# Kernel tuning notes

Measured on AMD Instinct MI355X. Metric: run time of the kernel, lower is better.

The kernel has to match this reference:

```python
import jax, jax.numpy as jnp
import numpy as np
from functools import partial

B, H, W = 2, 480, 480
C, HALF = 32, 16
L, WN, PAD = 4, 20, 20

def gelu(x):
    return jax.nn.gelu(x, approximate=False)

def setup_inputs() -> dict:
    key = jax.random.key(0)
    ks = jax.random.split(key, 24)
    scale = 1.0 / (C * C)
    d = {}
    d["input_data"] = jax.random.normal(ks[0], (B, H, W, 1), jnp.float32)
    d["src_data"] = jax.random.normal(ks[1], (B, H, W, 3), jnp.float32)
    # input lifting MLP: sizes [5, 16, 32]
    d["in_w1"] = jax.random.normal(ks[2], (5, HALF), jnp.float32) * 0.1
    d["in_b1"] = jnp.zeros((HALF,), jnp.float32)
    d["in_w2"] = jax.random.normal(ks[3], (HALF, C), jnp.float32) * 0.1
    d["in_b2"] = jnp.zeros((C,), jnp.float32)
    # eps lifting MLP: sizes [3, 16, 32]
    d["eps_w1"] = jax.random.normal(ks[4], (3, HALF), jnp.float32) * 0.1
    d["eps_b1"] = jnp.zeros((HALF,), jnp.float32)
    d["eps_w2"] = jax.random.normal(ks[5], (HALF, C), jnp.float32) * 0.1
    d["eps_b2"] = jnp.zeros((C,), jnp.float32)
    # Fourier layer params, stacked over L layers
    d["fw1"] = jax.random.uniform(ks[6], (L, C, C, WN, WN, 2), jnp.float32) * scale
    d["fw2"] = jax.random.uniform(ks[7], (L, C, C, WN, WN, 2), jnp.float32) * scale
    d["conv_w"] = jax.random.normal(ks[8], (L, C, C), jnp.float32) * 0.05
    d["conv_b"] = jnp.zeros((L, C), jnp.float32)
    # projection MLP: sizes [32, 16, 2]
    d["proj_w1"] = jax.random.normal(ks[9], (C, HALF), jnp.float32) * 0.1
    d["proj_b1"] = jnp.zeros((HALF,), jnp.float32)
    d["proj_w2"] = jax.random.normal(ks[10], (HALF, 2), jnp.float32) * 0.1
    d["proj_b2"] = jnp.zeros((2,), jnp.float32)
    # mask conv 3x3, 1->1 channel
    d["mask_w"] = jax.random.normal(ks[11], (1, 1, 3, 3), jnp.float32) * 0.1
    d["mask_b"] = jnp.zeros((1,), jnp.float32)
    return d

def _grid(b, h, w):
    gx = jnp.broadcast_to(jnp.linspace(0.0, 1.0, h, dtype=jnp.float32)[None, :, None, None], (b, h, w, 1))
    gy = jnp.broadcast_to(jnp.linspace(0.0, 1.0, w, dtype=jnp.float32)[None, None, :, None], (b, h, w, 1))
    return jnp.concatenate([gx, gy], axis=-1)

def _mlp(x, w1, b1, w2, b2):
    # FCLayer(gelu) then FCLayer(linear)
    return gelu(x @ w1 + b1) @ w2 + b2

def _fourier_conv(x, x_eps, w1, w2):
    # x, x_eps: [B, C, Hp, Wp]
    hp, wp = x.shape[-2], x.shape[-1]
    xf = jnp.fft.rfft2(x * x_eps)                       # [B,C,Hp,Wp//2+1] complex
    xr = jnp.stack([xf.real, xf.imag], axis=-1)         # [B,C,Hp,Wp//2+1,2]
    lo = jnp.einsum('bixyz,ioxyz->boxyz', xr[:, :, :WN, :WN, :], w1)
    hi = jnp.einsum('bixyz,ioxyz->boxyz', xr[:, :, -WN:, :WN, :], w2)
    out = jnp.zeros((x.shape[0], w1.shape[1], hp, wp // 2 + 1, 2), jnp.float32)
    out = out.at[:, :, :WN, :WN, :].set(lo)
    out = out.at[:, :, -WN:, :WN, :].set(hi)
    return jnp.fft.irfft2(out[..., 0] + 1j * out[..., 1], s=(hp, wp))

def _forward(input_data, src_data, in_w1, in_b1, in_w2, in_b2,
             eps_w1, eps_b1, eps_w2, eps_b2, fw1, fw2, conv_w, conv_b,
             proj_w1, proj_b1, proj_w2, proj_b2, mask_w, mask_b):
    b, h, w = input_data.shape[0], input_data.shape[1], input_data.shape[2]
    grid = _grid(b, h, w)
    x_in = jnp.concatenate([src_data, grid], axis=-1)       # [B,H,W,5]
    x_eps = jnp.concatenate([input_data, grid], axis=-1)    # [B,H,W,3]
    field = src_data[..., 1:]                               # [B,H,W,2]

    a = _mlp(x_in, in_w1, in_b1, in_w2, in_b2)              # [B,H,W,C]
    a = jnp.transpose(a, (0, 3, 1, 2))                      # [B,C,H,W]
    a = jnp.pad(a, ((0, 0), (0, 0), (0, PAD), (0, PAD)))    # [B,C,H+P,W+P]
    e = _mlp(x_eps, eps_w1, eps_b1, eps_w2, eps_b2)
    e = jnp.transpose(e, (0, 3, 1, 2))
    e = jnp.pad(e, ((0, 0), (0, 0), (0, PAD), (0, PAD)))

    for l in range(L):
        x1 = _fourier_conv(a, e, fw1[l], fw2[l])
        x2 = jnp.einsum('bihw,oi->bohw', a, conv_w[l]) + conv_b[l][None, :, None, None]
        a = x1 + x2
        if l < L - 1:
            a = gelu(a)

    pred = a[..., :-PAD, :-PAD]                             # [B,C,H,W]
    pred = jnp.transpose(pred, (0, 2, 3, 1))                # [B,H,W,C]
    pred = _mlp(pred, proj_w1, proj_b1, proj_w2, proj_b2)   # [B,H,W,2]

    xm = jnp.transpose(input_data, (0, 3, 1, 2))            # [B,1,H,W]
    mask = jax.lax.conv_general_dilated(xm, mask_w, (1, 1), 'SAME',
                                        dimension_numbers=('NCHW', 'OIHW', 'NCHW'))
    mask = mask + mask_b[None, :, None, None]
    mask = jnp.transpose(mask, (0, 2, 3, 1))                # [B,H,W,1] -> broadcasts over 2
    return field * mask + pred

def reference(input_data, src_data, in_w1, in_b1, in_w2, in_b2,
              eps_w1, eps_b1, eps_w2, eps_b2, fw1, fw2, conv_w, conv_b,
              proj_w1, proj_b1, proj_w2, proj_b2, mask_w, mask_b):
    return _forward(input_data, src_data, in_w1, in_b1, in_w2, in_b2,
                    eps_w1, eps_b1, eps_w2, eps_b2, fw1, fw2, conv_w, conv_b,
                    proj_w1, proj_b1, proj_w2, proj_b2, mask_w, mask_b)
```

## Files before the change

kernel.cpp:

```cpp
#include <hip/hip_runtime.h>
#include <hip/hip_bf16.h>

#define BD 2
#define HD 480
#define WD 480
#define CD 32
#define HALFD 16
#define WND 20
#define NP 500
#define PLANE (HD*WD)
#define TWO_PI_OVER_NP 0.012566370614359172954f

typedef __attribute__((ext_vector_type(8))) short bf16x8;
typedef __attribute__((ext_vector_type(4))) float f32x4;

__device__ __forceinline__ float gelu_f(float x) {
    return 0.5f * x * (1.0f + erff(x * 0.70710678118654752f));
}
__device__ __forceinline__ float bfbits2f(short s) {
    unsigned u = ((unsigned)(unsigned short)s) << 16;
    return __uint_as_float(u);
}
__device__ __forceinline__ short bf16s(float v) {
    __hip_bfloat16 b = __float2bfloat16(v);
    return *reinterpret_cast<short*>(&b);
}
__device__ __forceinline__ unsigned pk2(float a, float b) {
    return (unsigned)(unsigned short)bf16s(a) | ((unsigned)(unsigned short)bf16s(b) << 16);
}

__global__ void __launch_bounds__(256) k_ae(
    const float* src, const float* inp,
    const float* iw1, const float* ib1,
    const float* iw2, const float* ib2,
    const float* ew1, const float* eb1,
    const float* ew2, const float* eb2,
    __hip_bfloat16* A, __hip_bfloat16* E)
{
    __shared__ float s_iw1[80], s_ib1[16];
    __shared__ float s_ew1[48], s_eb1[16];
    __shared__ __align__(16) __hip_bfloat16 s_hidA[256 * 24];
    __shared__ __align__(16) __hip_bfloat16 s_hidE[256 * 24];
    __shared__ __align__(16) __hip_bfloat16 s_out[32 * 264];

    int tid = threadIdx.x;
    int lane = tid & 63, wv = tid >> 6;

    if (tid < 80) s_iw1[tid] = iw1[tid];
    if (tid >= 96 && tid < 112) s_ib1[tid - 96] = ib1[tid - 96];
    if (tid >= 128 && tid < 176) s_ew1[tid - 128] = ew1[tid - 128];
    if (tid >= 192 && tid < 208) s_eb1[tid - 192] = eb1[tid - 192];

    int c0 = lane & 15, kg = lane >> 4;
    bf16x8 bIn[2], bEps[2];
    float biasIn[2], biasEps[2];
    #pragma unroll
    for (int nt = 0; nt < 2; nt++) {
        int c = nt * 16 + c0;
        #pragma unroll
        for (int j = 0; j < 8; j++) {
            int k = kg * 8 + j;
            bIn[nt][j]  = (k < 16) ? bf16s(iw2[k * 32 + c]) : (short)0;
            bEps[nt][j] = (k < 16) ? bf16s(ew2[k * 32 + c]) : (short)0;
        }
        biasIn[nt]  = ib2[c];
        biasEps[nt] = eb2[c];
    }
    __syncthreads();

    int gid = blockIdx.x * 256 + tid;
    int b = gid / PLANE;
    int r = gid % PLANE;
    int h = r / WD, w = r % WD;
    float gx = (float)h * (1.0f / 479.0f);
    float gy = (float)w * (1.0f / 479.0f);
    float s0 = src[(size_t)gid * 3 + 0];
    float s1 = src[(size_t)gid * 3 + 1];
    float s2 = src[(size_t)gid * 3 + 2];
    float xi = inp[gid];

    {
        unsigned pk[8];
        #pragma unroll
        for (int j = 0; j < 16; j += 2) {
            float v0 = s_ib1[j]     + s0 * s_iw1[j]     + s1 * s_iw1[16 + j]
                     + s2 * s_iw1[32 + j]     + gx * s_iw1[48 + j]     + gy * s_iw1[64 + j];
            float v1 = s_ib1[j + 1] + s0 * s_iw1[j + 1] + s1 * s_iw1[16 + j + 1]
                     + s2 * s_iw1[32 + j + 1] + gx * s_iw1[48 + j + 1] + gy * s_iw1[64 + j + 1];
            pk[j >> 1] = pk2(gelu_f(v0), gelu_f(v1));
        }
        uint4* d = reinterpret_cast<uint4*>(&s_hidA[tid * 24]);
        d[0] = make_uint4(pk[0], pk[1], pk[2], pk[3]);
        d[1] = make_uint4(pk[4], pk[5], pk[6], pk[7]);
        #pragma unroll
        for (int j = 0; j < 16; j += 2) {
            float v0 = s_eb1[j]     + xi * s_ew1[j]     + gx * s_ew1[16 + j]     + gy * s_ew1[32 + j];
            float v1 = s_eb1[j + 1] + xi * s_ew1[j + 1] + gx * s_ew1[16 + j + 1] + gy * s_ew1[32 + j + 1];
            pk[j >> 1] = pk2(gelu_f(v0), gelu_f(v1));
        }
        uint4* d2 = reinterpret_cast<uint4*>(&s_hidE[tid * 24]);
        d2[0] = make_uint4(pk[0], pk[1], pk[2], pk[3]);
        d2[1] = make_uint4(pk[4], pk[5], pk[6], pk[7]);
    }
    __syncthreads();

    int r0 = (blockIdx.x % 900) * 256;

    #pragma unroll
    for (int pass = 0; pass < 2; pass++) {
        const __hip_bfloat16* hid = pass ? s_hidE : s_hidA;
        #pragma unroll
        for (int t = 0; t < 4; t++) {
            int tile = wv * 4 + t;
            bf16x8 av = {0, 0, 0, 0, 0, 0, 0, 0};
            if (kg < 2)
                av = *reinterpret_cast<const bf16x8*>(&hid[(tile * 16 + c0) * 24 + kg * 8]);
            #pragma unroll
            for (int nt = 0; nt < 2; nt++) {
                f32x4 acc = {0.f, 0.f, 0.f, 0.f};
                bf16x8 bv = pass ? bEps[nt] : bIn[nt];
                acc = __builtin_amdgcn_mfma_f32_16x16x32_bf16(av, bv, acc, 0, 0, 0);
                float bias = pass ? biasEps[nt] : biasIn[nt];
                int ch = nt * 16 + c0;
                int px = tile * 16 + kg * 4;
                unsigned w0 = pk2(acc[0] + bias, acc[1] + bias);
                unsigned w1 = pk2(acc[2] + bias, acc[3] + bias);
                *reinterpret_cast<uint2*>(&s_out[ch * 264 + px]) = make_uint2(w0, w1);
            }
        }
        __syncthreads();
        __hip_bfloat16* dst = (pass ? E : A) + (size_t)b * CD * PLANE + r0;
        #pragma unroll
        for (int i = 0; i < 4; i++) {
            int idx = tid + i * 256;
            int ch = idx >> 5, chunk = idx & 31;
            uint4 v = *reinterpret_cast<const uint4*>(&s_out[ch * 264 + chunk * 8]);
            *reinterpret_cast<uint4*>(&dst[(size_t)ch * PLANE + chunk * 8]) = v;
        }
        __syncthreads();
    }
}

__global__ void k_tables(__hip_bfloat16* T) {
    int e = blockIdx.x * 256 + threadIdx.x;
    if (e >= 435 * 512) return;
    int tile = e >> 9, r = e & 511;
    int lane = r >> 3, j = r & 7;
    float v = 0.0f;
    if (tile < 45) {
        int kt = tile / 3, nt = tile % 3;
        int k = kt * 32 + ((lane >> 4) << 3) + j;
        int n = nt * 16 + (lane & 15);
        if (n < 40) {
            int ky = n >> 1;
            int idx = (k * ky) % NP;
            float ang = (float)idx * TWO_PI_OVER_NP;
            v = (n & 1) ? -sinf(ang) : cosf(ang);
        }
    } else if (tile < 105) {
        int t2 = tile - 45;
        int nt = t2 >> 1, kt = t2 & 1;
        int kk = kt * 32 + ((lane >> 4) << 3) + j;
        int w = nt * 16 + (lane & 15);
        if (kk < 40) {
            int ky = kk >> 1;
            int idx = (ky * w) % NP;
            float ang = (float)idx * TWO_PI_OVER_NP;
            v = (kk & 1) ? -sinf(ang) : cosf(ang);
        }
    } else if (tile < 255) {
        int t2 = tile - 105;
        int kt = t2 / 5, nt = t2 % 5;
        int k = kt * 32 + ((lane >> 4) << 3) + j;
        int n = nt * 16 + (lane & 15);
        int hh = k >> 1, ri = k & 1;
        int kxi = n >> 1, part = n & 1;
        int kx = (kxi < 20) ? kxi : kxi + 460;
        int idx = (kx * hh) % NP;
        float ang = (float)idx * TWO_PI_OVER_NP;
        float c = cosf(ang), s = sinf(ang);
        v = (part == 0) ? (ri == 0 ? c : s) : (ri == 0 ? -s : c);
    } else {
        int t2 = tile - 255;
        int nt = t2 / 3, kt = t2 % 3;
        int k = kt * 32 + ((lane >> 4) << 3) + j;
        int n = nt * 16 + (lane & 15);
        if (k < 80) {
            int kxi = k >> 1, ri = k & 1;
            int hh = n >> 1, part = n & 1;
            int kx = (kxi < 20) ? kxi : kxi + 460;
            int idx = (kx * hh) % NP;
            float ang = (float)idx * TWO_PI_OVER_NP;
            float c = cosf(ang), s = sinf(ang);
            v = (part == 0) ? (ri == 0 ? c : -s) : (ri == 0 ? s : c);
        }
    }
    T[e] = __float2bfloat16(v);
}

__global__ void __launch_bounds__(256) k_F1m(
    const __hip_bfloat16* A, const __hip_bfloat16* E,
    const __hip_bfloat16* Twig, __hip_bfloat16* Y1)
{
    int wv = threadIdx.x >> 6, lane = threadIdx.x & 63;
    int task = blockIdx.x * 4 + wv;
    int bh = task / 6, rem = task % 6;
    int mt = rem & 1, nt = rem >> 1;
    int b = bh / HD, h = bh % HD;
    int c = mt * 16 + (lane & 15);
    int koff = (lane >> 4) << 3;
    size_t base = ((size_t)(b * 32 + c)) * PLANE + (size_t)h * WD + koff;
    const __hip_bfloat16* arow = A + base;
    const __hip_bfloat16* erow = E + base;
    f32x4 acc = {0.f, 0.f, 0.f, 0.f};
    #pragma unroll
    for (int kt = 0; kt < 15; kt++) {
        bf16x8 av = *reinterpret_cast<const bf16x8*>(arow + kt * 32);
        bf16x8 ev = *reinterpret_cast<const bf16x8*>(erow + kt * 32);
        bf16x8 gv;
        #pragma unroll
        for (int j = 0; j < 8; j++)
            gv[j] = bf16s(bfbits2f(av[j]) * bfbits2f(ev[j]));
        bf16x8 bv = *reinterpret_cast<const bf16x8*>(Twig + (((kt * 3 + nt) << 9) + lane * 8));
        acc = __builtin_amdgcn_mfma_f32_16x16x32_bf16(gv, bv, acc, 0, 0, 0);
    }
    int n = nt * 16 + (lane & 15);
    if (n < 40) {
        int ky = n >> 1, part = n & 1;
        int crow = mt * 16 + ((lane >> 4) << 2);
        #pragma unroll
        for (int r = 0; r < 4; r++) {
            int cc = crow + r;
            Y1[((((size_t)(b * 32 + cc)) * WND + ky) * HD + h) * 2 + part] =
                __float2bfloat16(acc[r]);
        }
    }
}

__global__ void __launch_bounds__(256) k_F2m(
    const __hip_bfloat16* Y1, const __hip_bfloat16* Tf2, float* Y2)
{
    int wv = threadIdx.x >> 6, lane = threadIdx.x & 63;
    int task = blockIdx.x * 4 + wv;
    int mt = task / 5, nt = task % 5;
    int row = mt * 16 + (lane & 15);
    int koff = (lane >> 4) << 3;
    const __hip_bfloat16* arow = Y1 + (size_t)row * 960 + koff;
    f32x4 acc = {0.f, 0.f, 0.f, 0.f};
    #pragma unroll
    for (int kt = 0; kt < 30; kt++) {
        bf16x8 av = *reinterpret_cast<const bf16x8*>(arow + kt * 32);
        bf16x8 bv = *reinterpret_cast<const bf16x8*>(Tf2 + (((kt * 5 + nt) << 9) + lane * 8));
        acc = __builtin_amdgcn_mfma_f32_16x16x32_bf16(av, bv, acc, 0, 0, 0);
    }
    int n = nt * 16 + (lane & 15);
    int mb = mt * 16 + ((lane >> 4) << 2);
    #pragma unroll
    for (int r = 0; r < 4; r++)
        Y2[(size_t)(mb + r) * 80 + n] = acc[r];
}

__global__ void __launch_bounds__(256) k_mix(
    const float* Y2, __hip_bfloat16* Zb,
    const float* fw1, const float* fw2, int l)
{
    int gid = blockIdx.x * 256 + threadIdx.x;
    int col = gid % 96;
    int row = gid / 96;
    if (col >= 80) { Zb[gid] = __float2bfloat16(0.0f); return; }
    int ky = row % 20;
    int oc = (row / 20) % 32;
    int b = row / 640;
    int z = col & 1;
    int kxi = col >> 1;
    const float* wp;
    int x;
    if (kxi < 20) { wp = fw1; x = kxi; } else { wp = fw2; x = kxi - 20; }
    size_t wbase = ((((size_t)(l * 32) * 32 + oc) * 20 + x) * 20 + ky) * 2 + z;
    const float* y2 = Y2 + ((size_t)b * 32 * 20 + ky) * 80 + kxi * 2 + z;
    float acc = 0.f;
    for (int i = 0; i < 32; i++) {
        float yv = y2[(size_t)i * 1600];
        float wv = wp[wbase + (size_t)i * 25600];
        acc += yv * wv;
    }
    Zb[gid] = __float2bfloat16(acc);
}

__global__ void __launch_bounds__(256) k_I1m(
    const __hip_bfloat16* Zb, const __hip_bfloat16* Ti1, __hip_bfloat16* U)
{
    int wv = threadIdx.x >> 6, lane = threadIdx.x & 63;
    int task = blockIdx.x * 4 + wv;
    int mt = task / 60, nt = task % 60;
    int row = mt * 16 + (lane & 15);
    int koff = (lane >> 4) << 3;
    const __hip_bfloat16* arow = Zb + (size_t)row * 96 + koff;
    f32x4 acc = {0.f, 0.f, 0.f, 0.f};
    #pragma unroll
    for (int kt = 0; kt < 3; kt++) {
        bf16x8 av = *reinterpret_cast<const bf16x8*>(arow + kt * 32);
        bf16x8 bv = *reinterpret_cast<const bf16x8*>(Ti1 + (((nt * 3 + kt) << 9) + lane * 8));
        acc = __builtin_amdgcn_mfma_f32_16x16x32_bf16(av, bv, acc, 0, 0, 0);
    }
    int n = nt * 16 + (lane & 15);
    int mb = mt * 16 + ((lane >> 4) << 2);
    #pragma unroll
    for (int r = 0; r < 4; r++)
        U[(size_t)(mb + r) * 960 + n] = __float2bfloat16(acc[r]);
}

__global__ void __launch_bounds__(512) k_I2F1(
    const __hip_bfloat16* U, __hip_bfloat16* A,
    const __hip_bfloat16* E,
    const float* convw, const float* convb,
    const __hip_bfloat16* TinvF, const __hip_bfloat16* Twig,
    __hip_bfloat16* Y1, int l)
{
    __shared__ __align__(16) __hip_bfloat16 sBf[30 * 512];
    __shared__ __align__(16) __hip_bfloat16 sUf[4 * 512];
    __shared__ __align__(16) __hip_bfloat16 sWf[2 * 512];
    __shared__ __align__(16) __hip_bfloat16 sA[32 * 488];
    __shared__ float sB[CD];
    int tid = threadIdx.x;
    int b = blockIdx.x / HD;
    int h = blockIdx.x % HD;
    if (tid < CD) sB[tid] = convb[l * CD + tid];
    for (int t = tid; t < 2048; t += 512) {
        int j = t & 7, lane = (t >> 3) & 63, ktmt = t >> 9;
        int mt = ktmt >> 1, kt = ktmt & 1;
        int oc = mt * 16 + (lane & 15);
        int kk = kt * 32 + ((lane >> 4) << 3) + j;
        float v = 0.f;
        if (kk < 40) {
            int ky = kk >> 1;
            __hip_bfloat162 u = reinterpret_cast<const __hip_bfloat162*>(U)
                [(((size_t)b * CD + oc) * WND + ky) * HD + h];
            float sc = (ky == 0 ? 1.0f : 2.0f) * (1.0f / 250000.0f);
            v = ((kk & 1) ? __bfloat162float(u.y) : __bfloat162float(u.x)) * sc;
        }
        sUf[t] = __float2bfloat16(v);
    }
    for (int t = tid; t < 1024; t += 512) {
        int j = t & 7, lane = (t >> 3) & 63, mt = t >> 9;
        int oc = mt * 16 + (lane & 15);
        int ic = ((lane >> 4) << 3) + j;
        sWf[t] = __float2bfloat16(convw[(size_t)l * CD * CD + oc * CD + ic]);
    }
    {
        const unsigned short* Ab = reinterpret_cast<const unsigned short*>(
            A + (size_t)b * CD * PLANE + (size_t)h * WD);
        for (int w = tid; w < WD; w += 512) {
            unsigned short vals[32];
            #pragma unroll
            for (int ic = 0; ic < 32; ic++)
                vals[ic] = Ab[(size_t)ic * PLANE + w];
            int nt = w >> 4, lw = w & 15;
            #pragma unroll
            for (int q = 0; q < 4; q++) {
                uint4 pk;
                pk.x = (unsigned)vals[8 * q + 0] | ((unsigned)vals[8 * q + 1] << 16);
                pk.y = (unsigned)vals[8 * q + 2] | ((unsigned)vals[8 * q + 3] << 16);
                pk.z = (unsigned)vals[8 * q + 4] | ((unsigned)vals[8 * q + 5] << 16);
                pk.w = (unsigned)vals[8 * q + 6] | ((unsigned)vals[8 * q + 7] << 16);
                *reinterpret_cast<uint4*>(&sBf[(nt << 9) + (((q << 4) | lw) << 3)]) = pk;
            }
        }
    }
    __syncthreads();
    int wv = tid >> 6, lane = tid & 63;
    for (int t = wv; t < 60; t += 8) {
        int mt = t & 1, nt = t >> 1;
        f32x4 acc = {0.f, 0.f, 0.f, 0.f};
        #pragma unroll
        for (int kt = 0; kt < 2; kt++) {
            bf16x8 av = *reinterpret_cast<const bf16x8*>(&sUf[((mt * 2 + kt) << 9) + lane * 8]);
            bf16x8 bv = *reinterpret_cast<const bf16x8*>(TinvF + (((nt * 2 + kt) << 9) + lane * 8));
            acc = __builtin_amdgcn_mfma_f32_16x16x32_bf16(av, bv, acc, 0, 0, 0);
        }
        bf16x8 av2 = *reinterpret_cast<const bf16x8*>(&sWf[(mt << 9) + lane * 8]);
        bf16x8 bv2 = *reinterpret_cast<const bf16x8*>(&sBf[(nt << 9) + lane * 8]);
        acc = __builtin_amdgcn_mfma_f32_16x16x32_bf16(av2, bv2, acc, 0, 0, 0);
        int w = nt * 16 + (lane & 15);
        int ocb = mt * 16 + ((lane >> 4) << 2);
        #pragma unroll
        for (int r = 0; r < 4; r++) {
            float v = gelu_f(acc[r] + sB[ocb + r]);
            short sv = bf16s(v);
            sA[(ocb + r) * 488 + w] = *reinterpret_cast<__hip_bfloat16*>(&sv);
            A[((size_t)b * CD + (ocb + r)) * PLANE + (size_t)h * WD + w] =
                *reinterpret_cast<__hip_bfloat16*>(&sv);
        }
    }
    __syncthreads();
    int c0 = lane & 15, kg = lane >> 4;
    for (int t = wv; t < 6; t += 8) {
        int mt = t & 1, nt = t >> 1;
        int c = mt * 16 + c0;
        const __hip_bfloat16* erow =
            E + ((size_t)(b * 32 + c)) * PLANE + (size_t)h * WD + (kg << 3);
        const __hip_bfloat16* albase = &sA[c * 488 + (kg << 3)];
        f32x4 acc = {0.f, 0.f, 0.f, 0.f};
        #pragma unroll
        for (int kt = 0; kt < 15; kt++) {
            bf16x8 av = *reinterpret_cast<const bf16x8*>(albase + kt * 32);
            bf16x8 ev = *reinterpret_cast<const bf16x8*>(erow + kt * 32);
            bf16x8 gv;
            #pragma unroll
            for (int j = 0; j < 8; j++)
                gv[j] = bf16s(bfbits2f(av[j]) * bfbits2f(ev[j]));
            bf16x8 bv = *reinterpret_cast<const bf16x8*>(Twig + (((kt * 3 + nt) << 9) + lane * 8));
            acc = __builtin_amdgcn_mfma_f32_16x16x32_bf16(gv, bv, acc, 0, 0, 0);
        }
        int n = nt * 16 + c0;
        if (n < 40) {
            int ky = n >> 1, part = n & 1;
            int crow = mt * 16 + (kg << 2);
            #pragma unroll
            for (int r = 0; r < 4; r++) {
                int cc = crow + r;
                Y1[((((size_t)(b * 32 + cc)) * WND + ky) * HD + h) * 2 + part] =
                    __float2bfloat16(acc[r]);
            }
        }
    }
}

__global__ void __launch_bounds__(512) k_I2out(
    const __hip_bfloat16* U, const __hip_bfloat16* A,
    const float* convw, const float* convb,
    const __hip_bfloat16* TinvF,
    const float* inp, const float* src,
    const float* pw1, const float* pb1,
    const float* pw2, const float* pb2,
    const float* mw, const float* mb,
    float* out, int l)
{
    __shared__ __align__(16) __hip_bfloat16 sBf[30 * 512];
    __shared__ __align__(16) __hip_bfloat16 sUf[4 * 512];
    __shared__ __align__(16) __hip_bfloat16 sWf[2 * 512];
    __shared__ __align__(16) __hip_bfloat16 sA[32 * 488];
    __shared__ float sB[CD];
    __shared__ float sW1[CD * HALFD], sB1[HALFD], sW2[HALFD * 2], sB2[2], sM[9], sMB[1];
    int tid = threadIdx.x;
    int b = blockIdx.x / HD;
    int h = blockIdx.x % HD;
    if (tid < CD) sB[tid] = convb[l * CD + tid];
    sW1[tid] = pw1[tid];
    if (tid >= 32 && tid < 48) sB1[tid - 32] = pb1[tid - 32];
    if (tid >= 64 && tid < 96) sW2[tid - 64] = pw2[tid - 64];
    if (tid >= 96 && tid < 98) sB2[tid - 96] = pb2[tid - 96];
    if (tid >= 128 && tid < 137) sM[tid - 128] = mw[tid - 128];
    if (tid == 160) sMB[0] = mb[0];
    for (int t = tid; t < 2048; t += 512) {
        int j = t & 7, lane = (t >> 3) & 63, ktmt = t >> 9;
        int mt = ktmt >> 1, kt = ktmt & 1;
        int oc = mt * 16 + (lane & 15);
        int kk = kt * 32 + ((lane >> 4) << 3) + j;
        float v = 0.f;
        if (kk < 40) {
            int ky = kk >> 1;
            __hip_bfloat162 u = reinterpret_cast<const __hip_bfloat162*>(U)
                [(((size_t)b * CD + oc) * WND + ky) * HD + h];
            float sc = (ky == 0 ? 1.0f : 2.0f) * (1.0f / 250000.0f);
            v = ((kk & 1) ? __bfloat162float(u.y) : __bfloat162float(u.x)) * sc;
        }
        sUf[t] = __float2bfloat16(v);
    }
    for (int t = tid; t < 1024; t += 512) {
        int j = t & 7, lane = (t >> 3) & 63, mt = t >> 9;
        int oc = mt * 16 + (lane & 15);
        int ic = ((lane >> 4) << 3) + j;
        sWf[t] = __float2bfloat16(convw[(size_t)l * CD * CD + oc * CD + ic]);
    }
    {
        const unsigned short* Ab = reinterpret_cast<const unsigned short*>(
            A + (size_t)b * CD * PLANE + (size_t)h * WD);
        for (int w = tid; w < WD; w += 512) {
            unsigned short vals[32];
            #pragma unroll
            for (int ic = 0; ic < 32; ic++)
                vals[ic] = Ab[(size_t)ic * PLANE + w];
            int nt = w >> 4, lw = w & 15;
            #pragma unroll
            for (int q = 0; q < 4; q++) {
                uint4 pk;
                pk.x = (unsigned)vals[8 * q + 0] | ((unsigned)vals[8 * q + 1] << 16);
                pk.y = (unsigned)vals[8 * q + 2] | ((unsigned)vals[8 * q + 3] << 16);
                pk.z = (unsigned)vals[8 * q + 4] | ((unsigned)vals[8 * q + 5] << 16);
                pk.w = (unsigned)vals[8 * q + 6] | ((unsigned)vals[8 * q + 7] << 16);
                *reinterpret_cast<uint4*>(&sBf[(nt << 9) + (((q << 4) | lw) << 3)]) = pk;
            }
        }
    }
    __syncthreads();
    int wv = tid >> 6, lane = tid & 63;
    for (int t = wv; t < 60; t += 8) {
        int mt = t & 1, nt = t >> 1;
        f32x4 acc = {0.f, 0.f, 0.f, 0.f};
        #pragma unroll
        for (int kt = 0; kt < 2; kt++) {
            bf16x8 av = *reinterpret_cast<const bf16x8*>(&sUf[((mt * 2 + kt) << 9) + lane * 8]);
            bf16x8 bv = *reinterpret_cast<const bf16x8*>(TinvF + (((nt * 2 + kt) << 9) + lane * 8));
            acc = __builtin_amdgcn_mfma_f32_16x16x32_bf16(av, bv, acc, 0, 0, 0);
        }
        bf16x8 av2 = *reinterpret_cast<const bf16x8*>(&sWf[(mt << 9) + lane * 8]);
        bf16x8 bv2 = *reinterpret_cast<const bf16x8*>(&sBf[(nt << 9) + lane * 8]);
        acc = __builtin_amdgcn_mfma_f32_16x16x32_bf16(av2, bv2, acc, 0, 0, 0);
        int w = nt * 16 + (lane & 15);
        int ocb = mt * 16 + ((lane >> 4) << 2);
        #pragma unroll
        for (int r = 0; r < 4; r++) {
            short sv = bf16s(acc[r] + sB[ocb + r]);
            sA[(ocb + r) * 488 + w] = *reinterpret_cast<__hip_bfloat16*>(&sv);
        }
    }
    __syncthreads();
    for (int w = tid; w < WD; w += 512) {
        float av[32];
        #pragma unroll
        for (int i = 0; i < 32; i++) av[i] = bfbits2f(
            *reinterpret_cast<const short*>(&sA[i * 488 + w]));
        float hid[16];
        #pragma unroll
        for (int j = 0; j < 16; j++) {
            float v = sB1[j];
            #pragma unroll
            for (int i = 0; i < 32; i++) v += av[i] * sW1[i * 16 + j];
            hid[j] = gelu_f(v);
        }
        float p0 = sB2[0], p1 = sB2[1];
        #pragma unroll
        for (int j = 0; j < 16; j++) { p0 += hid[j] * sW2[j * 2]; p1 += hid[j] * sW2[j * 2 + 1]; }
        float m = sMB[0];
        #pragma unroll
        for (int dh = 0; dh < 3; dh++) {
            int hh = h + dh - 1;
            #pragma unroll
            for (int dw = 0; dw < 3; dw++) {
                int ww = w + dw - 1;
                if (hh >= 0 && hh < HD && ww >= 0 && ww < WD)
                    m += inp[(size_t)b * PLANE + (size_t)hh * WD + ww] * sM[dh * 3 + dw];
            }
        }
        size_t gid = (size_t)b * PLANE + (size_t)h * WD + w;
        float f0 = src[gid * 3 + 1];
        float f1 = src[gid * 3 + 2];
        out[gid * 2 + 0] = f0 * m + p0;
        out[gid * 2 + 1] = f1 * m + p1;
    }
}

extern "C" void kernel_launch(void* const* d_in, const int* in_sizes, int n_in,
                              void* d_out, int out_size, void* d_ws, size_t ws_size,
                              hipStream_t stream) {
    const float* inp = (const float*)d_in[0];
    const float* src = (const float*)d_in[1];
    const float* iw1 = (const float*)d_in[2];
    const float* ib1 = (const float*)d_in[3];
    const float* iw2 = (const float*)d_in[4];
    const float* ib2 = (const float*)d_in[5];
    const float* ew1 = (const float*)d_in[6];
    const float* eb1 = (const float*)d_in[7];
    const float* ew2 = (const float*)d_in[8];
    const float* eb2 = (const float*)d_in[9];
    const float* fw1 = (const float*)d_in[10];
    const float* fw2 = (const float*)d_in[11];
    const float* cw  = (const float*)d_in[12];
    const float* cb  = (const float*)d_in[13];
    const float* pw1 = (const float*)d_in[14];
    const float* pb1 = (const float*)d_in[15];
    const float* pw2 = (const float*)d_in[16];
    const float* pb2 = (const float*)d_in[17];
    const float* mw  = (const float*)d_in[18];
    const float* mb  = (const float*)d_in[19];

    const size_t NA = (size_t)BD * CD * PLANE;
    __hip_bfloat16* A   = (__hip_bfloat16*)d_ws;
    __hip_bfloat16* E   = A + NA;
    __hip_bfloat16* Y1U = E + NA;
    float* Y2 = (float*)(Y1U + (size_t)BD * CD * WND * HD * 2);
    __hip_bfloat16* Zb = (__hip_bfloat16*)(Y2 + 1280 * 80);
    __hip_bfloat16* Tbl   = Zb + 1280 * 96;
    __hip_bfloat16* Twig  = Tbl;
    __hip_bfloat16* TinvF = Twig + 45 * 512;
    __hip_bfloat16* Tf2   = TinvF + 60 * 512;
    __hip_bfloat16* Ti1   = Tf2 + 150 * 512;

    k_tables<<<870, 256, 0, stream>>>(Tbl);
    k_ae<<<1800, 256, 0, stream>>>(src, inp, iw1, ib1, iw2, ib2,
                                   ew1, eb1, ew2, eb2, A, E);

    k_F1m<<<1440, 256, 0, stream>>>(A, E, Twig, Y1U);
    for (int l = 0; l < 4; l++) {
        k_F2m<<<100, 256, 0, stream>>>(Y1U, Tf2, Y2);
        k_mix<<<480, 256, 0, stream>>>(Y2, Zb, fw1, fw2, l);
        k_I1m<<<1200, 256, 0, stream>>>(Zb, Ti1, Y1U);
        if (l < 3)
            k_I2F1<<<BD * HD, 512, 0, stream>>>(Y1U, A, E, cw, cb, TinvF, Twig,
                                                Y1U, l);
        else
            k_I2out<<<BD * HD, 512, 0, stream>>>(Y1U, A, cw, cb, TinvF,
                                                 inp, src, pw1, pb1, pw2, pb2,
                                                 mw, mb, (float*)d_out, l);
    }
}
```

Measured before the change: 411.7 us.

## Load activation B-operand directly from global, drop staging buffer, coalesce A writeback

Removes the shared-memory staging buffer sBf in both layer kernels and loads the MFMA B operand for the pointwise conv directly from global A per lane. In k_I2F1 the scattered per-element global store of the new activation is replaced by a coalesced 16-byte copy from shared memory after the barrier, which also avoids overwriting A while other waves may still be reading it. In k_I2out, sA becomes a transposed, padded sAT layout so the per-pixel MLP reads contiguous channels, and both kernels get a min-blocks launch bound hint. The gain is lower LDS use and higher occupancy, at the cost of strided 2-byte global loads for the B operand.

New measurement: 407.2 us. Within noise of the previous version (-1.1%).

```diff
diff --git a/kernel.cpp b/kernel.cpp
--- a/kernel.cpp
+++ b/kernel.cpp
@@ -310,14 +310,13 @@
         U[(size_t)(mb + r) * 960 + n] = __float2bfloat16(acc[r]);
 }
 
-__global__ void __launch_bounds__(512) k_I2F1(
+__global__ void __launch_bounds__(512, 8) k_I2F1(
     const __hip_bfloat16* U, __hip_bfloat16* A,
     const __hip_bfloat16* E,
     const float* convw, const float* convb,
     const __hip_bfloat16* TinvF, const __hip_bfloat16* Twig,
     __hip_bfloat16* Y1, int l)
 {
-    __shared__ __align__(16) __hip_bfloat16 sBf[30 * 512];
     __shared__ __align__(16) __hip_bfloat16 sUf[4 * 512];
     __shared__ __align__(16) __hip_bfloat16 sWf[2 * 512];
     __shared__ __align__(16) __hip_bfloat16 sA[32 * 488];
@@ -347,28 +346,11 @@
         int ic = ((lane >> 4) << 3) + j;
         sWf[t] = __float2bfloat16(convw[(size_t)l * CD * CD + oc * CD + ic]);
     }
-    {
-        const unsigned short* Ab = reinterpret_cast<const unsigned short*>(
-            A + (size_t)b * CD * PLANE + (size_t)h * WD);
-        for (int w = tid; w < WD; w += 512) {
-            unsigned short vals[32];
-            #pragma unroll
-            for (int ic = 0; ic < 32; ic++)
-                vals[ic] = Ab[(size_t)ic * PLANE + w];
-            int nt = w >> 4, lw = w & 15;
-            #pragma unroll
-            for (int q = 0; q < 4; q++) {
-                uint4 pk;
-                pk.x = (unsigned)vals[8 * q + 0] | ((unsigned)vals[8 * q + 1] << 16);
-                pk.y = (unsigned)vals[8 * q + 2] | ((unsigned)vals[8 * q + 3] << 16);
-                pk.z = (unsigned)vals[8 * q + 4] | ((unsigned)vals[8 * q + 5] << 16);
-                pk.w = (unsigned)vals[8 * q + 6] | ((unsigned)vals[8 * q + 7] << 16);
-                *reinterpret_cast<uint4*>(&sBf[(nt << 9) + (((q << 4) | lw) << 3)]) = pk;
-            }
-        }
-    }
     __syncthreads();
     int wv = tid >> 6, lane = tid & 63;
+    int c0 = lane & 15, kg = lane >> 4;
+    const unsigned short* Ap = reinterpret_cast<const unsigned short*>(A)
+        + (size_t)b * CD * PLANE + (size_t)h * WD;
     for (int t = wv; t < 60; t += 8) {
         int mt = t & 1, nt = t >> 1;
         f32x4 acc = {0.f, 0.f, 0.f, 0.f};
@@ -379,21 +361,28 @@
             acc = __builtin_amdgcn_mfma_f32_16x16x32_bf16(av, bv, acc, 0, 0, 0);
         }
         bf16x8 av2 = *reinterpret_cast<const bf16x8*>(&sWf[(mt << 9) + lane * 8]);
-        bf16x8 bv2 = *reinterpret_cast<const bf16x8*>(&sBf[(nt << 9) + lane * 8]);
+        bf16x8 bv2;
+        #pragma unroll
+        for (int j = 0; j < 8; j++)
+            bv2[j] = (short)Ap[(size_t)(kg * 8 + j) * PLANE + nt * 16 + c0];
         acc = __builtin_amdgcn_mfma_f32_16x16x32_bf16(av2, bv2, acc, 0, 0, 0);
-        int w = nt * 16 + (lane & 15);
-        int ocb = mt * 16 + ((lane >> 4) << 2);
+        int w = nt * 16 + c0;
+        int ocb = mt * 16 + (kg << 2);
         #pragma unroll
         for (int r = 0; r < 4; r++) {
-            float v = gelu_f(acc[r] + sB[ocb + r]);
-            short sv = bf16s(v);
+            short sv = bf16s(gelu_f(acc[r] + sB[ocb + r]));
             sA[(ocb + r) * 488 + w] = *reinterpret_cast<__hip_bfloat16*>(&sv);
-            A[((size_t)b * CD + (ocb + r)) * PLANE + (size_t)h * WD + w] =
-                *reinterpret_cast<__hip_bfloat16*>(&sv);
         }
     }
     __syncthreads();
-    int c0 = lane & 15, kg = lane >> 4;
+    {
+        __hip_bfloat16* Adst = A + (size_t)b * CD * PLANE + (size_t)h * WD;
+        for (int t = tid; t < 32 * 60; t += 512) {
+            int row = t / 60, chunk = t % 60;
+            uint4 v = *reinterpret_cast<const uint4*>(&sA[row * 488 + chunk * 8]);
+            *reinterpret_cast<uint4*>(&Adst[(size_t)row * PLANE + chunk * 8]) = v;
+        }
+    }
     for (int t = wv; t < 6; t += 8) {
         int mt = t & 1, nt = t >> 1;
         int c = mt * 16 + c0;
@@ -426,7 +415,7 @@
     }
 }
 
-__global__ void __launch_bounds__(512) k_I2out(
+__global__ void __launch_bounds__(512, 8) k_I2out(
     const __hip_bfloat16* U, const __hip_bfloat16* A,
     const float* convw, const float* convb,
     const __hip_bfloat16* TinvF,
@@ -436,10 +425,9 @@
     const float* mw, const float* mb,
     float* out, int l)
 {
-    __shared__ __align__(16) __hip_bfloat16 sBf[30 * 512];
     __shared__ __align__(16) __hip_bfloat16 sUf[4 * 512];
     __shared__ __align__(16) __hip_bfloat16 sWf[2 * 512];
-    __shared__ __align__(16) __hip_bfloat16 sA[32 * 488];
+    __shared__ __hip_bfloat16 sAT[WD * 33];
     __shared__ float sB[CD];
     __shared__ float sW1[CD * HALFD], sB1[HALFD], sW2[HALFD * 2], sB2[2], sM[9], sMB[1];
     int tid = threadIdx.x;
@@ -473,28 +461,11 @@
         int ic = ((lane >> 4) << 3) + j;
         sWf[t] = __float2bfloat16(convw[(size_t)l * CD * CD + oc * CD + ic]);
     }
-    {
-        const unsigned short* Ab = reinterpret_cast<const unsigned short*>(
-            A + (size_t)b * CD * PLANE + (size_t)h * WD);
-        for (int w = tid; w < WD; w += 512) {
-            unsigned short vals[32];
-            #pragma unroll
-            for (int ic = 0; ic < 32; ic++)
-                vals[ic] = Ab[(size_t)ic * PLANE + w];
-            int nt = w >> 4, lw = w & 15;
-            #pragma unroll
-            for (int q = 0; q < 4; q++) {
-                uint4 pk;
-                pk.x = (unsigned)vals[8 * q + 0] | ((unsigned)vals[8 * q + 1] << 16);
-                pk.y = (unsigned)vals[8 * q + 2] | ((unsigned)vals[8 * q + 3] << 16);
-                pk.z = (unsigned)vals[8 * q + 4] | ((unsigned)vals[8 * q + 5] << 16);
-                pk.w = (unsigned)vals[8 * q + 6] | ((unsigned)vals[8 * q + 7] << 16);
-                *reinterpret_cast<uint4*>(&sBf[(nt << 9) + (((q << 4) | lw) << 3)]) = pk;
-            }
-        }
-    }
     __syncthreads();
     int wv = tid >> 6, lane = tid & 63;
+    int c0 = lane & 15, kg = lane >> 4;
+    const unsigned short* Ap = reinterpret_cast<const unsigned short*>(A)
+        + (size_t)b * CD * PLANE + (size_t)h * WD;
     for (int t = wv; t < 60; t += 8) {
         int mt = t & 1, nt = t >> 1;
         f32x4 acc = {0.f, 0.f, 0.f, 0.f};
@@ -505,14 +476,17 @@
             acc = __builtin_amdgcn_mfma_f32_16x16x32_bf16(av, bv, acc, 0, 0, 0);
         }
         bf16x8 av2 = *reinterpret_cast<const bf16x8*>(&sWf[(mt << 9) + lane * 8]);
-        bf16x8 bv2 = *reinterpret_cast<const bf16x8*>(&sBf[(nt << 9) + lane * 8]);
+        bf16x8 bv2;
+        #pragma unroll
+        for (int j = 0; j < 8; j++)
+            bv2[j] = (short)Ap[(size_t)(kg * 8 + j) * PLANE + nt * 16 + c0];
         acc = __builtin_amdgcn_mfma_f32_16x16x32_bf16(av2, bv2, acc, 0, 0, 0);
-        int w = nt * 16 + (lane & 15);
-        int ocb = mt * 16 + ((lane >> 4) << 2);
+        int w = nt * 16 + c0;
+        int ocb = mt * 16 + (kg << 2);
         #pragma unroll
         for (int r = 0; r < 4; r++) {
             short sv = bf16s(acc[r] + sB[ocb + r]);
-            sA[(ocb + r) * 488 + w] = *reinterpret_cast<__hip_bfloat16*>(&sv);
+            sAT[w * 33 + (ocb + r)] = *reinterpret_cast<__hip_bfloat16*>(&sv);
         }
     }
     __syncthreads();
@@ -520,7 +494,7 @@
         float av[32];
         #pragma unroll
         for (int i = 0; i < 32; i++) av[i] = bfbits2f(
-            *reinterpret_cast<const short*>(&sA[i * 488 + w]));
+            *reinterpret_cast<const short*>(&sAT[w * 33 + i]));
         float hid[16];
         #pragma unroll
         for (int j = 0; j < 16; j++) {
```
